# Kernel tuning notes

Hardware: AMD Instinct MI355X
Metric: run time of the kernel (lower is better)

## Reference

```python
import jax, jax.numpy as jnp
import numpy as np

N_NODES = 100000
N_EDGES = 500000
D = 128


def setup_inputs() -> dict:
    key = jax.random.key(0)
    ks = jax.random.split(key, 6)
    x = jax.random.normal(ks[0], (N_NODES, D), dtype=jnp.float32)
    edge_index = jax.random.randint(ks[1], (2, N_EDGES), 0, N_NODES, dtype=jnp.int64)
    edge_label = jax.random.randint(ks[2], (N_EDGES,), 0, 2, dtype=jnp.int64)
    # MLP params (dim_in -> dim_in, 2 layers, has_act=True, has_bias=True)
    scale = 1.0 / np.sqrt(D)
    W1 = jax.random.normal(ks[3], (D, D), dtype=jnp.float32) * scale
    b1 = jnp.zeros((D,), dtype=jnp.float32)
    W2 = jax.random.normal(ks[4], (D, D), dtype=jnp.float32) * scale
    b2 = jnp.zeros((D,), dtype=jnp.float32)
    return {"x": x, "edge_index": edge_index, "edge_label": edge_label,
            "W1": W1, "b1": b1, "W2": W2, "b2": b2}


def reference(x, edge_index, edge_label, W1, b1, W2, b2):
    # post-MP MLP on all node features (has_act=True -> ReLU after each layer)
    h = jax.nn.relu(x @ W1 + b1)          # [N, D]
    h = jax.nn.relu(h @ W2 + b2)          # [N, D]
    # gather endpoints: batch.x[edge_index] -> [2, E, D]
    v1 = h[edge_index[0]]                  # [E, D]
    v2 = h[edge_index[1]]                  # [E, D]
    # dot decode: sum(v1 * v2, dim=-1)
    pred = jnp.sum(v1 * v2, axis=-1)       # [E]
    return pred, edge_label
```

## Files before the change

### kernel.cpp

```cpp
#include <hip/hip_runtime.h>

typedef __attribute__((ext_vector_type(8))) short short8;
typedef __attribute__((ext_vector_type(4))) short short4v;
typedef __attribute__((ext_vector_type(4))) float floatx4;

#define D 128
#define NWAVES 4
#define GRID_MLP 512

__device__ __forceinline__ unsigned short f2bf(float f) {
  unsigned u = __float_as_uint(f);
  u += 0x7FFFu + ((u >> 16) & 1u);
  return (unsigned short)(u >> 16);
}

__device__ __forceinline__ void stageW(const float* __restrict__ W,
                                       unsigned short* __restrict__ sW, int tid) {
  const int n = tid & 127;
  const int tg = tid >> 7;
  #pragma unroll
  for (int iter = 0; iter < 16; ++iter) {
    const int k0 = iter * 8 + tg * 4;
    float w0 = W[(k0 + 0) * D + n];
    float w1 = W[(k0 + 1) * D + n];
    float w2 = W[(k0 + 2) * D + n];
    float w3 = W[(k0 + 3) * D + n];
    short4v p;
    p[0] = (short)f2bf(w0); p[1] = (short)f2bf(w1);
    p[2] = (short)f2bf(w2); p[3] = (short)f2bf(w3);
    const int idx = n * D + (((k0 >> 3) ^ (n & 15)) << 3) + (k0 & 7);
    *(short4v*)&sW[idx] = p;
  }
}

__global__ __launch_bounds__(256) void mlp_fused(
    const float* __restrict__ x, const float* __restrict__ W1,
    const float* __restrict__ b1, const float* __restrict__ W2,
    const float* __restrict__ b2, unsigned short* __restrict__ h,
    const int* __restrict__ elabel, float* __restrict__ out,
    int nNodes, int ntiles, int E) {
  __shared__ unsigned short sW1[D * D];
  __shared__ unsigned short sW2[D * D];
  __shared__ unsigned short sH[NWAVES][16 * D];
  const int tid = threadIdx.x;
  const int wave = tid >> 6, lane = tid & 63;
  const int quad = lane >> 4, l16 = lane & 15;

  for (int le = blockIdx.x * 256 + tid; le < E; le += GRID_MLP * 256)
    out[E + le] = (float)elabel[le];

  stageW(W1, sW1, tid);
  stageW(W2, sW2, tid);
  __syncthreads();

  float bias1[8], bias2[8];
  #pragma unroll
  for (int n0 = 0; n0 < 8; ++n0) { bias1[n0] = b1[n0 * 16 + l16]; bias2[n0] = b2[n0 * 16 + l16]; }

  unsigned short* mysH = sH[wave];

  for (int t = blockIdx.x * NWAVES + wave; t < ntiles; t += GRID_MLP * NWAVES) {
    const int m = t * 16 + l16;
    const bool mv = (m < nNodes);
    float4 xf[8];
    const float* xp = x + (size_t)m * D + quad * 8;
    #pragma unroll
    for (int kk = 0; kk < 4; ++kk) {
      if (mv) {
        xf[2 * kk]     = *(const float4*)(xp + kk * 32);
        xf[2 * kk + 1] = *(const float4*)(xp + kk * 32 + 4);
      } else {
        xf[2 * kk] = make_float4(0, 0, 0, 0);
        xf[2 * kk + 1] = make_float4(0, 0, 0, 0);
      }
    }
    floatx4 acc[8];
    #pragma unroll
    for (int n0 = 0; n0 < 8; ++n0) acc[n0] = (floatx4){0.f, 0.f, 0.f, 0.f};
    #pragma unroll
    for (int kk = 0; kk < 4; ++kk) {
      const float4 f0 = xf[2 * kk], f1 = xf[2 * kk + 1];
      short8 a;
      a[0] = (short)f2bf(f0.x); a[1] = (short)f2bf(f0.y);
      a[2] = (short)f2bf(f0.z); a[3] = (short)f2bf(f0.w);
      a[4] = (short)f2bf(f1.x); a[5] = (short)f2bf(f1.y);
      a[6] = (short)f2bf(f1.z); a[7] = (short)f2bf(f1.w);
      #pragma unroll
      for (int n0 = 0; n0 < 8; ++n0) {
        short8 b = *(const short8*)&sW1[(n0 * 16 + l16) * D + (((kk * 4 + quad) ^ l16) << 3)];
        acc[n0] = __builtin_amdgcn_mfma_f32_16x16x32_bf16(a, b, acc[n0], 0, 0, 0);
      }
    }
    #pragma unroll
    for (int n0 = 0; n0 < 8; ++n0) {
      #pragma unroll
      for (int r = 0; r < 4; ++r) {
        float v = acc[n0][r] + bias1[n0];
        v = v > 0.f ? v : 0.f;
        const int row = quad * 4 + r;
        const int g = 2 * n0 + (l16 >> 3);
        mysH[row * D + (((g ^ row) & 15) << 3) + (l16 & 7)] = f2bf(v);
      }
    }
    short8 af[4];
    #pragma unroll
    for (int kk = 0; kk < 4; ++kk)
      af[kk] = *(const short8*)&mysH[l16 * D + ((((kk * 4 + quad) ^ l16) & 15) << 3)];
    #pragma unroll
    for (int n0 = 0; n0 < 8; ++n0) acc[n0] = (floatx4){0.f, 0.f, 0.f, 0.f};
    #pragma unroll
    for (int kk = 0; kk < 4; ++kk) {
      #pragma unroll
      for (int n0 = 0; n0 < 8; ++n0) {
        short8 b = *(const short8*)&sW2[(n0 * 16 + l16) * D + (((kk * 4 + quad) ^ l16) << 3)];
        acc[n0] = __builtin_amdgcn_mfma_f32_16x16x32_bf16(af[kk], b, acc[n0], 0, 0, 0);
      }
    }
    #pragma unroll
    for (int n0 = 0; n0 < 8; ++n0) {
      #pragma unroll
      for (int r = 0; r < 4; ++r) {
        float v = acc[n0][r] + bias2[n0];
        v = v > 0.f ? v : 0.f;
        const int row = quad * 4 + r;
        const int g = 2 * n0 + (l16 >> 3);
        mysH[row * D + (((g ^ row) & 15) << 3) + (l16 & 7)] = f2bf(v);
      }
    }
    #pragma unroll
    for (int i = 0; i < 4; ++i) {
      const int row = i * 4 + quad;
      short8 vrow = *(const short8*)&mysH[row * D + (((l16 ^ row) & 15) << 3)];
      const int g = t * 16 + row;
      if (g < nNodes) *(short8*)&h[(size_t)g * D + l16 * 8] = vrow;
    }
  }
}

__device__ __forceinline__ float dot2bf(unsigned a, unsigned b, float acc) {
  float a0 = __uint_as_float(a << 16);
  float a1 = __uint_as_float(a & 0xFFFF0000u);
  float b0 = __uint_as_float(b << 16);
  float b1 = __uint_as_float(b & 0xFFFF0000u);
  acc = fmaf(a0, b0, acc);
  acc = fmaf(a1, b1, acc);
  return acc;
}

__device__ __forceinline__ float edge_dot(const uint4& a, const uint4& b) {
  float acc = 0.f;
  acc = dot2bf(a.x, b.x, acc);
  acc = dot2bf(a.y, b.y, acc);
  acc = dot2bf(a.z, b.z, acc);
  acc = dot2bf(a.w, b.w, acc);
  acc += __shfl_xor(acc, 8);
  acc += __shfl_xor(acc, 4);
  acc += __shfl_xor(acc, 2);
  acc += __shfl_xor(acc, 1);
  return acc;
}

__global__ __launch_bounds__(256) void edge_kernel(
    const unsigned short* __restrict__ h2, const int* __restrict__ eidx,
    float* __restrict__ out, int E) {
  const int sub = threadIdx.x & 15;
  const int grp = (blockIdx.x * 256 + threadIdx.x) >> 4;
  const int e0 = grp * 8;
  if (e0 + 8 <= E) {
    const int4 s0 = *(const int4*)&eidx[e0];
    const int4 s1 = *(const int4*)&eidx[e0 + 4];
    const int4 t0 = *(const int4*)&eidx[E + e0];
    const int4 t1 = *(const int4*)&eidx[E + e0 + 4];
    int s[8] = {s0.x, s0.y, s0.z, s0.w, s1.x, s1.y, s1.z, s1.w};
    int d[8] = {t0.x, t0.y, t0.z, t0.w, t1.x, t1.y, t1.z, t1.w};
    uint4 va[8], vb[8];
    #pragma unroll
    for (int i = 0; i < 8; ++i) {
      va[i] = *(const uint4*)(h2 + (size_t)s[i] * D + sub * 8);
      vb[i] = *(const uint4*)(h2 + (size_t)d[i] * D + sub * 8);
    }
    #pragma unroll
    for (int i = 0; i < 8; ++i) {
      float acc = edge_dot(va[i], vb[i]);
      if (sub == 0) out[e0 + i] = acc;
    }
  } else if (e0 < E) {
    for (int e = e0; e < E; ++e) {
      const int s = eidx[e];
      const int d = eidx[E + e];
      const uint4 ua = *(const uint4*)(h2 + (size_t)s * D + sub * 8);
      const uint4 ub = *(const uint4*)(h2 + (size_t)d * D + sub * 8);
      float acc = edge_dot(ua, ub);
      if (sub == 0) out[e] = acc;
    }
  }
}

extern "C" void kernel_launch(void* const* d_in, const int* in_sizes, int n_in,
                              void* d_out, int out_size, void* d_ws, size_t ws_size,
                              hipStream_t stream) {
  const float* x  = (const float*)d_in[0];
  const int* eidx = (const int*)d_in[1];
  const int* elab = (const int*)d_in[2];
  const float* W1 = (const float*)d_in[3];
  const float* b1 = (const float*)d_in[4];
  const float* W2 = (const float*)d_in[5];
  const float* b2 = (const float*)d_in[6];
  float* out = (float*)d_out;

  const int nNodes = in_sizes[0] / D;
  const int E = in_sizes[2];
  const int ntiles = (nNodes + 15) / 16;

  unsigned short* h = (unsigned short*)d_ws;

  mlp_fused<<<GRID_MLP, 256, 0, stream>>>(x, W1, b1, W2, b2, h, elab, out,
                                          nNodes, ntiles, E);

  const int edgeBlocks = (E + 127) / 128;
  edge_kernel<<<edgeBlocks, 256, 0, stream>>>(h, eidx, out, E);
}
```

Before: 140.5 us.

## Software-pipeline x loads in MLP and use persistent double-buffered edge gather

The MLP loop now double-buffers x tiles in registers, loading the next tile before computing the current one, which hides global-load latency behind MFMA work. The edge kernel becomes a persistent grid of 1024 blocks. Each 16-lane group walks quads of edges, prefetching the next quad's gathered rows while the current dot products are reduced. The label copy is vectorized to int4/float4. The cost is higher register pressure, which may lower occupancy, and the edge kernel now has fewer in-flight loads per thread (4 instead of 8 edges).

```diff
diff --git a/kernel.cpp b/kernel.cpp
--- a/kernel.cpp
+++ b/kernel.cpp
@@ -7,6 +7,8 @@
 #define D 128
 #define NWAVES 4
 #define GRID_MLP 512
+#define TSTRIDE (GRID_MLP * NWAVES)
+#define EDGE_BLOCKS 1024
 
 __device__ __forceinline__ unsigned short f2bf(float f) {
   unsigned u = __float_as_uint(f);
@@ -30,6 +32,89 @@
     p[2] = (short)f2bf(w2); p[3] = (short)f2bf(w3);
     const int idx = n * D + (((k0 >> 3) ^ (n & 15)) << 3) + (k0 & 7);
     *(short4v*)&sW[idx] = p;
+  }
+}
+
+__device__ __forceinline__ void load_x(const float* __restrict__ x, int t, int l16,
+                                       int quad, int nNodes, float4 xf[8]) {
+  const int m = t * 16 + l16;
+  if (m < nNodes) {
+    const float* xp = x + (size_t)m * D + quad * 8;
+    #pragma unroll
+    for (int kk = 0; kk < 4; ++kk) {
+      xf[2 * kk]     = *(const float4*)(xp + kk * 32);
+      xf[2 * kk + 1] = *(const float4*)(xp + kk * 32 + 4);
+    }
+  } else {
+    #pragma unroll
+    for (int i = 0; i < 8; ++i) xf[i] = make_float4(0.f, 0.f, 0.f, 0.f);
+  }
+}
+
+__device__ __forceinline__ void process_tile(
+    const float4 xf[8], int t, const unsigned short* __restrict__ sW1,
+    const unsigned short* __restrict__ sW2, unsigned short* __restrict__ mysH,
+    const float bias1[8], const float bias2[8], unsigned short* __restrict__ h,
+    int nNodes, int quad, int l16) {
+  floatx4 acc[8];
+  #pragma unroll
+  for (int n0 = 0; n0 < 8; ++n0) acc[n0] = (floatx4){0.f, 0.f, 0.f, 0.f};
+  #pragma unroll
+  for (int kk = 0; kk < 4; ++kk) {
+    const float4 f0 = xf[2 * kk], f1 = xf[2 * kk + 1];
+    short8 a;
+    a[0] = (short)f2bf(f0.x); a[1] = (short)f2bf(f0.y);
+    a[2] = (short)f2bf(f0.z); a[3] = (short)f2bf(f0.w);
+    a[4] = (short)f2bf(f1.x); a[5] = (short)f2bf(f1.y);
+    a[6] = (short)f2bf(f1.z); a[7] = (short)f2bf(f1.w);
+    #pragma unroll
+    for (int n0 = 0; n0 < 8; ++n0) {
+      short8 b = *(const short8*)&sW1[(n0 * 16 + l16) * D + (((kk * 4 + quad) ^ l16) << 3)];
+      acc[n0] = __builtin_amdgcn_mfma_f32_16x16x32_bf16(a, b, acc[n0], 0, 0, 0);
+    }
+  }
+  #pragma unroll
+  for (int n0 = 0; n0 < 8; ++n0) {
+    #pragma unroll
+    for (int r = 0; r < 4; ++r) {
+      float v = acc[n0][r] + bias1[n0];
+      v = v > 0.f ? v : 0.f;
+      const int row = quad * 4 + r;
+      const int g = 2 * n0 + (l16 >> 3);
+      mysH[row * D + (((g ^ row) & 15) << 3) + (l16 & 7)] = f2bf(v);
+    }
+  }
+  short8 af[4];
+  #pragma unroll
+  for (int kk = 0; kk < 4; ++kk)
+    af[kk] = *(const short8*)&mysH[l16 * D + ((((kk * 4 + quad) ^ l16) & 15) << 3)];
+  #pragma unroll
+  for (int n0 = 0; n0 < 8; ++n0) acc[n0] = (floatx4){0.f, 0.f, 0.f, 0.f};
+  #pragma unroll
+  for (int kk = 0; kk < 4; ++kk) {
+    #pragma unroll
+    for (int n0 = 0; n0 < 8; ++n0) {
+      short8 b = *(const short8*)&sW2[(n0 * 16 + l16) * D + (((kk * 4 + quad) ^ l16) << 3)];
+      acc[n0] = __builtin_amdgcn_mfma_f32_16x16x32_bf16(af[kk], b, acc[n0], 0, 0, 0);
+    }
+  }
+  #pragma unroll
+  for (int n0 = 0; n0 < 8; ++n0) {
+    #pragma unroll
+    for (int r = 0; r < 4; ++r) {
+      float v = acc[n0][r] + bias2[n0];
+      v = v > 0.f ? v : 0.f;
+      const int row = quad * 4 + r;
+      const int g = 2 * n0 + (l16 >> 3);
+      mysH[row * D + (((g ^ row) & 15) << 3) + (l16 & 7)] = f2bf(v);
+    }
+  }
+  #pragma unroll
+  for (int i = 0; i < 4; ++i) {
+    const int row = i * 4 + quad;
+    short8 vrow = *(const short8*)&mysH[row * D + (((l16 ^ row) & 15) << 3)];
+    const int g = t * 16 + row;
+    if (g < nNodes) *(short8*)&h[(size_t)g * D + l16 * 8] = vrow;
   }
 }
 
@@ -46,8 +131,15 @@
   const int wave = tid >> 6, lane = tid & 63;
   const int quad = lane >> 4, l16 = lane & 15;
 
-  for (int le = blockIdx.x * 256 + tid; le < E; le += GRID_MLP * 256)
-    out[E + le] = (float)elabel[le];
+  {
+    const int E4 = E & ~3;
+    for (int li = (blockIdx.x * 256 + tid) * 4; li < E4; li += GRID_MLP * 256 * 4) {
+      int4 lv = *(const int4*)&elabel[li];
+      float4 fv = make_float4((float)lv.x, (float)lv.y, (float)lv.z, (float)lv.w);
+      *(float4*)&out[E + li] = fv;
+    }
+    if (blockIdx.x == 0 && tid < (E & 3)) out[E + E4 + tid] = (float)elabel[E4 + tid];
+  }
 
   stageW(W1, sW1, tid);
   stageW(W2, sW2, tid);
@@ -59,80 +151,29 @@
 
   unsigned short* mysH = sH[wave];
 
-  for (int t = blockIdx.x * NWAVES + wave; t < ntiles; t += GRID_MLP * NWAVES) {
-    const int m = t * 16 + l16;
-    const bool mv = (m < nNodes);
-    float4 xf[8];
-    const float* xp = x + (size_t)m * D + quad * 8;
-    #pragma unroll
-    for (int kk = 0; kk < 4; ++kk) {
-      if (mv) {
-        xf[2 * kk]     = *(const float4*)(xp + kk * 32);
-        xf[2 * kk + 1] = *(const float4*)(xp + kk * 32 + 4);
-      } else {
-        xf[2 * kk] = make_float4(0, 0, 0, 0);
-        xf[2 * kk + 1] = make_float4(0, 0, 0, 0);
-      }
-    }
-    floatx4 acc[8];
-    #pragma unroll
-    for (int n0 = 0; n0 < 8; ++n0) acc[n0] = (floatx4){0.f, 0.f, 0.f, 0.f};
-    #pragma unroll
-    for (int kk = 0; kk < 4; ++kk) {
-      const float4 f0 = xf[2 * kk], f1 = xf[2 * kk + 1];
-      short8 a;
-      a[0] = (short)f2bf(f0.x); a[1] = (short)f2bf(f0.y);
-      a[2] = (short)f2bf(f0.z); a[3] = (short)f2bf(f0.w);
-      a[4] = (short)f2bf(f1.x); a[5] = (short)f2bf(f1.y);
-      a[6] = (short)f2bf(f1.z); a[7] = (short)f2bf(f1.w);
-      #pragma unroll
-      for (int n0 = 0; n0 < 8; ++n0) {
-        short8 b = *(const short8*)&sW1[(n0 * 16 + l16) * D + (((kk * 4 + quad) ^ l16) << 3)];
-        acc[n0] = __builtin_amdgcn_mfma_f32_16x16x32_bf16(a, b, acc[n0], 0, 0, 0);
-      }
-    }
-    #pragma unroll
-    for (int n0 = 0; n0 < 8; ++n0) {
-      #pragma unroll
-      for (int r = 0; r < 4; ++r) {
-        float v = acc[n0][r] + bias1[n0];
-        v = v > 0.f ? v : 0.f;
-        const int row = quad * 4 + r;
-        const int g = 2 * n0 + (l16 >> 3);
-        mysH[row * D + (((g ^ row) & 15) << 3) + (l16 & 7)] = f2bf(v);
-      }
-    }
-    short8 af[4];
-    #pragma unroll
-    for (int kk = 0; kk < 4; ++kk)
-      af[kk] = *(const short8*)&mysH[l16 * D + ((((kk * 4 + quad) ^ l16) & 15) << 3)];
-    #pragma unroll
-    for (int n0 = 0; n0 < 8; ++n0) acc[n0] = (floatx4){0.f, 0.f, 0.f, 0.f};
-    #pragma unroll
-    for (int kk = 0; kk < 4; ++kk) {
-      #pragma unroll
-      for (int n0 = 0; n0 < 8; ++n0) {
-        short8 b = *(const short8*)&sW2[(n0 * 16 + l16) * D + (((kk * 4 + quad) ^ l16) << 3)];
-        acc[n0] = __builtin_amdgcn_mfma_f32_16x16x32_bf16(af[kk], b, acc[n0], 0, 0, 0);
-      }
-    }
-    #pragma unroll
-    for (int n0 = 0; n0 < 8; ++n0) {
-      #pragma unroll
-      for (int r = 0; r < 4; ++r) {
-        float v = acc[n0][r] + bias2[n0];
-        v = v > 0.f ? v : 0.f;
-        const int row = quad * 4 + r;
-        const int g = 2 * n0 + (l16 >> 3);
-        mysH[row * D + (((g ^ row) & 15) << 3) + (l16 & 7)] = f2bf(v);
-      }
-    }
-    #pragma unroll
-    for (int i = 0; i < 4; ++i) {
-      const int row = i * 4 + quad;
-      short8 vrow = *(const short8*)&mysH[row * D + (((l16 ^ row) & 15) << 3)];
-      const int g = t * 16 + row;
-      if (g < nNodes) *(short8*)&h[(size_t)g * D + l16 * 8] = vrow;
+  float4 xfA[8], xfB[8];
+  int t = blockIdx.x * NWAVES + wave;
+  if (t < ntiles) {
+    load_x(x, t, l16, quad, nNodes, xfA);
+    while (true) {
+      int t2 = t + TSTRIDE;
+      if (t2 < ntiles) {
+        load_x(x, t2, l16, quad, nNodes, xfB);
+        process_tile(xfA, t, sW1, sW2, mysH, bias1, bias2, h, nNodes, quad, l16);
+        t = t2;
+      } else {
+        process_tile(xfA, t, sW1, sW2, mysH, bias1, bias2, h, nNodes, quad, l16);
+        break;
+      }
+      int t3 = t + TSTRIDE;
+      if (t3 < ntiles) {
+        load_x(x, t3, l16, quad, nNodes, xfA);
+        process_tile(xfB, t, sW1, sW2, mysH, bias1, bias2, h, nNodes, quad, l16);
+        t = t3;
+      } else {
+        process_tile(xfB, t, sW1, sW2, mysH, bias1, bias2, h, nNodes, quad, l16);
+        break;
+      }
     }
   }
 }
@@ -160,36 +201,71 @@
   return acc;
 }
 
+__device__ __forceinline__ void edge_load(const unsigned short* __restrict__ h2,
+                                          const int* __restrict__ eidx, int E,
+                                          int q, int sub, uint4 va[4], uint4 vb[4]) {
+  const int e0 = q * 4;
+  const int4 s = *(const int4*)&eidx[e0];
+  const int4 d = *(const int4*)&eidx[E + e0];
+  const size_t off = (size_t)(sub * 8);
+  va[0] = *(const uint4*)(h2 + (((size_t)(unsigned)s.x) << 7) + off);
+  va[1] = *(const uint4*)(h2 + (((size_t)(unsigned)s.y) << 7) + off);
+  va[2] = *(const uint4*)(h2 + (((size_t)(unsigned)s.z) << 7) + off);
+  va[3] = *(const uint4*)(h2 + (((size_t)(unsigned)s.w) << 7) + off);
+  vb[0] = *(const uint4*)(h2 + (((size_t)(unsigned)d.x) << 7) + off);
+  vb[1] = *(const uint4*)(h2 + (((size_t)(unsigned)d.y) << 7) + off);
+  vb[2] = *(const uint4*)(h2 + (((size_t)(unsigned)d.z) << 7) + off);
+  vb[3] = *(const uint4*)(h2 + (((size_t)(unsigned)d.w) << 7) + off);
+}
+
+__device__ __forceinline__ void edge_compute(const uint4 va[4], const uint4 vb[4],
+                                             int q, int sub, float* __restrict__ out) {
+  #pragma unroll
+  for (int i = 0; i < 4; ++i) {
+    float acc = edge_dot(va[i], vb[i]);
+    if (sub == 0) out[q * 4 + i] = acc;
+  }
+}
+
 __global__ __launch_bounds__(256) void edge_kernel(
     const unsigned short* __restrict__ h2, const int* __restrict__ eidx,
     float* __restrict__ out, int E) {
   const int sub = threadIdx.x & 15;
   const int grp = (blockIdx.x * 256 + threadIdx.x) >> 4;
-  const int e0 = grp * 8;
-  if (e0 + 8 <= E) {
-    const int4 s0 = *(const int4*)&eidx[e0];
-    const int4 s1 = *(const int4*)&eidx[e0 + 4];
-    const int4 t0 = *(const int4*)&eidx[E + e0];
-    const int4 t1 = *(const int4*)&eidx[E + e0 + 4];
-    int s[8] = {s0.x, s0.y, s0.z, s0.w, s1.x, s1.y, s1.z, s1.w};
-    int d[8] = {t0.x, t0.y, t0.z, t0.w, t1.x, t1.y, t1.z, t1.w};
-    uint4 va[8], vb[8];
-    #pragma unroll
-    for (int i = 0; i < 8; ++i) {
-      va[i] = *(const uint4*)(h2 + (size_t)s[i] * D + sub * 8);
-      vb[i] = *(const uint4*)(h2 + (size_t)d[i] * D + sub * 8);
-    }
-    #pragma unroll
-    for (int i = 0; i < 8; ++i) {
-      float acc = edge_dot(va[i], vb[i]);
-      if (sub == 0) out[e0 + i] = acc;
-    }
-  } else if (e0 < E) {
-    for (int e = e0; e < E; ++e) {
+  const int ngrp = (EDGE_BLOCKS * 256) >> 4;
+  const int nq = E >> 2;
+
+  uint4 vaA[4], vbA[4], vaB[4], vbB[4];
+  int q = grp;
+  if (q < nq) {
+    edge_load(h2, eidx, E, q, sub, vaA, vbA);
+    while (true) {
+      int q2 = q + ngrp;
+      if (q2 < nq) {
+        edge_load(h2, eidx, E, q2, sub, vaB, vbB);
+        edge_compute(vaA, vbA, q, sub, out);
+        q = q2;
+      } else {
+        edge_compute(vaA, vbA, q, sub, out);
+        break;
+      }
+      int q3 = q + ngrp;
+      if (q3 < nq) {
+        edge_load(h2, eidx, E, q3, sub, vaA, vbA);
+        edge_compute(vaB, vbB, q, sub, out);
+        q = q3;
+      } else {
+        edge_compute(vaB, vbB, q, sub, out);
+        break;
+      }
+    }
+  }
+  if (grp == ngrp - 1) {
+    for (int e = nq * 4; e < E; ++e) {
       const int s = eidx[e];
       const int d = eidx[E + e];
-      const uint4 ua = *(const uint4*)(h2 + (size_t)s * D + sub * 8);
-      const uint4 ub = *(const uint4*)(h2 + (size_t)d * D + sub * 8);
+      const uint4 ua = *(const uint4*)(h2 + (((size_t)(unsigned)s) << 7) + sub * 8);
+      const uint4 ub = *(const uint4*)(h2 + (((size_t)(unsigned)d) << 7) + sub * 8);
       float acc = edge_dot(ua, ub);
       if (sub == 0) out[e] = acc;
     }
@@ -216,7 +292,5 @@
 
   mlp_fused<<<GRID_MLP, 256, 0, stream>>>(x, W1, b1, W2, b2, h, elab, out,
                                           nNodes, ntiles, E);
-
-  const int edgeBlocks = (E + 127) / 128;
-  edge_kernel<<<edgeBlocks, 256, 0, stream>>>(h, eidx, out, E);
-}
+  edge_kernel<<<EDGE_BLOCKS, 256, 0, stream>>>(h, eidx, out, E);
+}
```

Result: slower. 150.4 us (+7.0%).
